# Kernel tuning notes

Measured on AMD Instinct MI355X. Metric: run time of the kernel, lower is better.

The kernel has to match this reference:

```python
import jax, jax.numpy as jnp
import numpy as np

N = 50000      # nodes
E = 1000000    # edges
NF = 5         # node_features
EF = 2         # edge_features
RS = 128       # rnn_size
RES = 32       # rnn_edge_size
H = 4          # heads
C = 16         # out_features
FIN = RS + RES # GAT in_channels
NEG_SLOPE = 0.2


def lstm_step(x, h, c, Wih, Whh, bih, bhh):
    # Single-step LSTM (torch gate order: i, f, g, o)
    g = x @ Wih.T + h @ Whh.T + bih + bhh
    i, f, gg, o = jnp.split(g, 4, axis=-1)
    i = jax.nn.sigmoid(i); f = jax.nn.sigmoid(f)
    gg = jnp.tanh(gg); o = jax.nn.sigmoid(o)
    c2 = f * c + i * gg
    return o * jnp.tanh(c2), c2


def setup_inputs() -> dict:
    key = jax.random.key(0)
    ks = jax.random.split(key, 20)
    p = lambda k, shape: (jax.random.normal(k, shape) * 0.1).astype(jnp.float32)
    return dict(
        x=jax.random.normal(ks[0], (N, NF), jnp.float32),
        edge_index=jax.random.randint(ks[1], (2, E), 0, N),
        edge_attr=jax.random.normal(ks[2], (E, EF), jnp.float32),
        h_node_h=p(ks[3], (N, RS)), h_node_c=p(ks[4], (N, RS)),
        h_edge_h=p(ks[5], (E, RES)), h_edge_c=p(ks[6], (E, RES)),
        Wih_n=p(ks[7], (4 * RS, NF)), Whh_n=p(ks[8], (4 * RS, RS)),
        bih_n=p(ks[9], (4 * RS,)), bhh_n=p(ks[10], (4 * RS,)),
        Wih_e=p(ks[11], (4 * RES, EF)), Whh_e=p(ks[12], (4 * RES, RES)),
        bih_e=p(ks[13], (4 * RES,)), bhh_e=p(ks[14], (4 * RES,)),
        W_gat=p(ks[15], (FIN, H * C)),
        att_src=p(ks[16], (H, C)), att_dst=p(ks[17], (H, C)),
        bias_gat=p(ks[18], (C,)),
    )


def reference(x, edge_index, edge_attr, h_node_h, h_node_c, h_edge_h, h_edge_c,
              Wih_n, Whh_n, bih_n, bhh_n, Wih_e, Whh_e, bih_e, bhh_e,
              W_gat, att_src, att_dst, bias_gat):
    n = x.shape[0]
    # --- edge history encoder: per-edge LSTM step + scatter-mean to dst nodes ---
    he, ce = lstm_step(edge_attr, h_edge_h, h_edge_c, Wih_e, Whh_e, bih_e, bhh_e)
    dst0 = edge_index[1]
    esum = jax.ops.segment_sum(he, dst0, num_segments=n)
    deg = jax.ops.segment_sum(jnp.ones((he.shape[0], 1), he.dtype), dst0, num_segments=n)
    edge_enc = esum / jnp.maximum(deg, 1.0)            # [N, RES]
    # --- node history encoder: per-node LSTM step ---
    hn, cn = lstm_step(x, h_node_h, h_node_c, Wih_n, Whh_n, bih_n, bhh_n)
    feat = jnp.concatenate([hn, edge_enc], axis=-1)    # [N, FIN]
    # --- GATConv (PyG v1 style, add_self_loops=True, concat=False) ---
    xl = (feat @ W_gat).reshape(n, H, C)               # [N, H, C]
    a_src = jnp.einsum('nhc,hc->nh', xl, att_src)
    a_dst = jnp.einsum('nhc,hc->nh', xl, att_dst)
    loops = jnp.arange(n)
    src = jnp.concatenate([edge_index[0], loops])
    dst = jnp.concatenate([edge_index[1], loops])
    alpha = jax.nn.leaky_relu(a_src[src] + a_dst[dst], NEG_SLOPE)  # [E+N, H]
    m = jax.ops.segment_max(alpha, dst, num_segments=n)
    ea = jnp.exp(alpha - m[dst])
    s = jax.ops.segment_sum(ea, dst, num_segments=n)
    w = ea / s[dst]                                     # segment softmax over dst
    out = jax.ops.segment_sum(xl[src] * w[:, :, None], dst, num_segments=n)  # [N,H,C]
    out = out.mean(axis=1) + bias_gat                   # concat=False -> head mean
    return (out, hn, cn, he, ce)
```

## Files before the change

### kernel.cpp

```cpp
#include <hip/hip_runtime.h>

#define CAP 128

typedef __attribute__((ext_vector_type(8))) short bf16x8;
typedef __attribute__((ext_vector_type(4))) float f32x4;

__device__ __forceinline__ float sigf(float x) {
    return __builtin_amdgcn_rcpf(1.0f + __expf(-x));
}
__device__ __forceinline__ float tanhfast(float x) {
    return 2.0f * __builtin_amdgcn_rcpf(1.0f + __expf(-2.0f * x)) - 1.0f;
}
__device__ __forceinline__ short bfr(float f) {
    unsigned u = __float_as_uint(f);
    unsigned r = (u + 0x7FFFu + ((u >> 16) & 1u)) >> 16;
    return (short)r;
}
__device__ __forceinline__ float bf2f(unsigned short u) {
    return __uint_as_float(((unsigned)u) << 16);
}
__device__ __forceinline__ bf16x8 cvt8(const float* p) {
    const float4* q = (const float4*)p;
    float4 u = q[0], v = q[1];
    bf16x8 r;
    r[0]=bfr(u.x); r[1]=bfr(u.y); r[2]=bfr(u.z); r[3]=bfr(u.w);
    r[4]=bfr(v.x); r[5]=bfr(v.y); r[6]=bfr(v.z); r[7]=bfr(v.w);
    return r;
}

__global__ void convert_kernel(
    const float* __restrict__ Whh_n, const float* __restrict__ Wih_n,
    const float* __restrict__ bih_n, const float* __restrict__ bhh_n,
    const float* __restrict__ Whh_e, const float* __restrict__ Wih_e,
    const float* __restrict__ bih_e, const float* __restrict__ bhh_e,
    const float* __restrict__ Wgat,
    unsigned short* __restrict__ WnF, unsigned short* __restrict__ WeF,
    unsigned short* __restrict__ WgF, int* __restrict__ cnt, int N)
{
    int i = blockIdx.x * 256 + threadIdx.x;
    if (i < N) cnt[i] = 0;
    if (i < 512 * 160) {
        int j = i & 7, unit = i >> 3;
        int lane = unit & 63, tk = unit >> 6;
        int tp = tk / 5, k4 = tk - tp * 5;
        int r = (tp & 3) * 128 + (tp >> 2) * 16 + (lane & 15);
        int k = k4 * 32 + (lane >> 4) * 8 + j;
        float v = (k < 128) ? Whh_n[r * 128 + k]
                : (k < 133) ? Wih_n[r * 5 + (k - 128)]
                : (k == 133) ? (bih_n[r] + bhh_n[r]) : 0.f;
        WnF[i] = (unsigned short)bfr(v);
    }
    if (i < 128 * 64) {
        int j = i & 7, unit = i >> 3;
        int lane = unit & 63, ts = unit >> 6;
        int t = ts >> 1, s = ts & 1;
        int r = t * 16 + (lane & 15);
        int k = s * 32 + (lane >> 4) * 8 + j;
        float v = (k < 32) ? Whh_e[r * 32 + k]
                : (k < 34) ? Wih_e[r * 2 + (k - 32)]
                : (k == 34) ? (bih_e[r] + bhh_e[r]) : 0.f;
        WeF[i] = (unsigned short)bfr(v);
    }
    if (i < 64 * 160) {
        int j = i & 7, unit = i >> 3;
        int lane = unit & 63, tk = unit >> 6;
        int t = tk / 5, k4 = tk - t * 5;
        int r = t * 16 + (lane & 15);
        int k = k4 * 32 + (lane >> 4) * 8 + j;
        WgF[i] = (unsigned short)bfr(Wgat[k * 64 + r]);
    }
}

__global__ void csr_fill_kernel(const int* __restrict__ dst, int* __restrict__ cnt,
                                int* __restrict__ eid, int E)
{
    int e = blockIdx.x * blockDim.x + threadIdx.x;
    if (e >= E) return;
    int d = dst[e];
    int k = atomicAdd(cnt + d, 1);
    if (k < CAP) eid[(size_t)d * CAP + k] = e;
}

__global__ __launch_bounds__(256, 4) void edge_lstm_mfma(
    const float* __restrict__ eattr, const float* __restrict__ h_in, const float* __restrict__ c_in,
    const unsigned short* __restrict__ WeF,
    float* __restrict__ he_out, float* __restrict__ ce_out, int E)
{
    __shared__ float Gall[4][16 * 132];
    __shared__ unsigned short Hall[4][16 * 40];
    const int lane = threadIdx.x & 63, wave = threadIdx.x >> 6;
    const int lr = lane & 15, lg = lane >> 4;
    const int tile = blockIdx.x * 4 + wave;
    if (tile * 16 >= E) return;
    float* G = Gall[wave];
    unsigned short* H = Hall[wave];

    const size_t dwbase = (size_t)tile * 512;
    const f32x4 hA = *(const f32x4*)(h_in + dwbase + lane * 4);
    const f32x4 hB = *(const f32x4*)(h_in + dwbase + 256 + lane * 4);
    const f32x4 cA = *(const f32x4*)(c_in + dwbase + lane * 4);
    const f32x4 cB = *(const f32x4*)(c_in + dwbase + 256 + lane * 4);
    float ea0 = 0.f, ea1 = 0.f;
    if (lg == 0) {
        ea0 = eattr[(size_t)(tile * 16 + lr) * 2];
        ea1 = eattr[(size_t)(tile * 16 + lr) * 2 + 1];
    }

    const bf16x8* Wv = (const bf16x8*)WeF;
    bf16x8 wa0[8], wa1[8];
    #pragma unroll
    for (int t = 0; t < 8; ++t) {
        wa0[t] = Wv[(t * 2 + 0) * 64 + lane];
        wa1[t] = Wv[(t * 2 + 1) * 64 + lane];
    }

    {
        const int e = lane >> 3, c4 = (lane & 7) * 4;
        ushort4 pa, pb;
        pa.x = (unsigned short)bfr(hA[0]); pa.y = (unsigned short)bfr(hA[1]);
        pa.z = (unsigned short)bfr(hA[2]); pa.w = (unsigned short)bfr(hA[3]);
        pb.x = (unsigned short)bfr(hB[0]); pb.y = (unsigned short)bfr(hB[1]);
        pb.z = (unsigned short)bfr(hB[2]); pb.w = (unsigned short)bfr(hB[3]);
        *(ushort4*)(H + e * 40 + c4)       = pa;
        *(ushort4*)(H + (8 + e) * 40 + c4) = pb;
    }
    bf16x8 b0 = *(const bf16x8*)(H + lr * 40 + lg * 8);
    bf16x8 b1 = {0,0,0,0,0,0,0,0};
    if (lg == 0) {
        b1[0] = bfr(ea0); b1[1] = bfr(ea1); b1[2] = (short)0x3F80;
    }

    f32x4 acc[8];
    #pragma unroll
    for (int t = 0; t < 8; ++t) {
        f32x4 v = {0, 0, 0, 0};
        v = __builtin_amdgcn_mfma_f32_16x16x32_bf16(wa0[t], b0, v, 0, 0, 0);
        v = __builtin_amdgcn_mfma_f32_16x16x32_bf16(wa1[t], b1, v, 0, 0, 0);
        acc[t] = v;
    }

    #pragma unroll
    for (int u = 0; u < 8; ++u) {
        const int col = (u >> 1) * 32 + (u & 1) * 16 + lg * 4;
        *(f32x4*)(G + lr * 132 + col) = acc[u];
    }

    const int e = lane >> 3, jq = (lane & 7) * 4;
    #pragma unroll
    for (int part = 0; part < 2; ++part) {
        const float* gr = G + (part * 8 + e) * 132;
        const f32x4 gi = *(const f32x4*)(gr + jq);
        const f32x4 gf = *(const f32x4*)(gr + 32 + jq);
        const f32x4 gg = *(const f32x4*)(gr + 64 + jq);
        const f32x4 go = *(const f32x4*)(gr + 96 + jq);
        const f32x4 cold = part ? cB : cA;
        f32x4 cres, hres;
        #pragma unroll
        for (int q = 0; q < 4; ++q) {
            float c2 = sigf(gf[q]) * cold[q] + sigf(gi[q]) * tanhfast(gg[q]);
            cres[q] = c2;
            hres[q] = sigf(go[q]) * tanhfast(c2);
        }
        __builtin_nontemporal_store(cres, (f32x4*)(ce_out + dwbase + part * 256 + lane * 4));
        *(f32x4*)(he_out + dwbase + part * 256 + lane * 4) = hres;
    }
}

__global__ __launch_bounds__(256) void node_lstm_mfma(
    const float* __restrict__ x, const float* __restrict__ h_in, const float* __restrict__ c_in,
    const unsigned short* __restrict__ WnF,
    float* __restrict__ hn_out, float* __restrict__ cn_out, int N)
{
    const int lane = threadIdx.x & 63, wave = threadIdx.x >> 6;
    const int nbase = blockIdx.x * 64 + wave * 16;
    if (nbase >= N) return;
    const int lr = lane & 15, lg = lane >> 4;
    const int node = nbase + lr;
    bf16x8 b[5];
    const float* hp = h_in + (size_t)node * 128 + lg * 8;
    b[0] = cvt8(hp); b[1] = cvt8(hp + 32); b[2] = cvt8(hp + 64); b[3] = cvt8(hp + 96);
    bf16x8 bx = {0,0,0,0,0,0,0,0};
    if (lg == 0) {
        const float* xp = x + (size_t)node * 5;
        bx[0]=bfr(xp[0]); bx[1]=bfr(xp[1]); bx[2]=bfr(xp[2]); bx[3]=bfr(xp[3]); bx[4]=bfr(xp[4]);
        bx[5] = (short)0x3F80;
    }
    b[4] = bx;
    const bf16x8* Wv = (const bf16x8*)WnF;
    #pragma unroll
    for (int u = 0; u < 8; ++u) {
        f32x4 acc[4];
        #pragma unroll
        for (int g = 0; g < 4; ++g) {
            const bf16x8* ap = Wv + (u * 4 + g) * 320 + lane;
            f32x4 v = {0, 0, 0, 0};
            #pragma unroll
            for (int k4 = 0; k4 < 5; ++k4)
                v = __builtin_amdgcn_mfma_f32_16x16x32_bf16(ap[k4 * 64], b[k4], v, 0, 0, 0);
            acc[g] = v;
        }
        const int jb = u * 16 + lg * 4;
        f32x4 cold = *(const f32x4*)(c_in + (size_t)node * 128 + jb);
        f32x4 cres, hres;
        #pragma unroll
        for (int q = 0; q < 4; ++q) {
            float c2 = sigf(acc[1][q]) * cold[q] + sigf(acc[0][q]) * tanhfast(acc[2][q]);
            cres[q] = c2;
            hres[q] = sigf(acc[3][q]) * tanhfast(c2);
        }
        __builtin_nontemporal_store(cres, (f32x4*)(cn_out + (size_t)node * 128 + jb));
        *(f32x4*)(hn_out + (size_t)node * 128 + jb) = hres;
    }
}

__global__ __launch_bounds__(256) void enc_gatxl_kernel(
    const int* __restrict__ cnt, const int* __restrict__ eid, const float* __restrict__ he,
    const float* __restrict__ hn, const unsigned short* __restrict__ WgF,
    const float* __restrict__ attS, const float* __restrict__ attD,
    unsigned short* __restrict__ xlb, float* __restrict__ asrc, float* __restrict__ adst, int N)
{
    __shared__ float encs[64 * 36];
    const int lane = threadIdx.x & 63, wave = threadIdx.x >> 6;
    const int nbase = blockIdx.x * 64 + wave * 16;
    if (nbase >= N) return;
    const int half = lane >> 5, hl = lane & 31;
    const int g4 = hl >> 3, l8 = hl & 7;
    for (int t = 0; t < 16; t += 2) {
        const int node = nbase + t + half;
        const int c = cnt[node];
        const int m = min(c, CAP);
        const int* el = eid + (size_t)node * CAP;
        f32x4 acc = {0, 0, 0, 0};
        for (int i = g4; i < m; i += 4)
            acc += *(const f32x4*)(he + (size_t)el[i] * 32 + l8 * 4);
        #pragma unroll
        for (int off = 8; off <= 16; off <<= 1) {
            acc[0] += __shfl_xor(acc[0], off);
            acc[1] += __shfl_xor(acc[1], off);
            acc[2] += __shfl_xor(acc[2], off);
            acc[3] += __shfl_xor(acc[3], off);
        }
        if (g4 == 0) {
            float inv = 1.0f / fmaxf((float)c, 1.0f);
            f32x4 r; r[0]=acc[0]*inv; r[1]=acc[1]*inv; r[2]=acc[2]*inv; r[3]=acc[3]*inv;
            *(f32x4*)(&encs[(wave * 16 + t + half) * 36 + l8 * 4]) = r;
        }
    }
    const int lr = lane & 15, lg = lane >> 4;
    const int node = nbase + lr;
    bf16x8 b[5];
    const float* hp = hn + (size_t)node * 128 + lg * 8;
    b[0] = cvt8(hp); b[1] = cvt8(hp + 32); b[2] = cvt8(hp + 64); b[3] = cvt8(hp + 96);
    b[4] = cvt8(&encs[(wave * 16 + lr) * 36 + lg * 8]);
    const bf16x8* Wv = (const bf16x8*)WgF;
    #pragma unroll
    for (int t = 0; t < 4; ++t) {
        const bf16x8* ap = Wv + t * 320 + lane;
        f32x4 v = {0, 0, 0, 0};
        #pragma unroll
        for (int k4 = 0; k4 < 5; ++k4)
            v = __builtin_amdgcn_mfma_f32_16x16x32_bf16(ap[k4 * 64], b[k4], v, 0, 0, 0);
        ushort4 pk;
        pk.x = (unsigned short)bfr(v[0]); pk.y = (unsigned short)bfr(v[1]);
        pk.z = (unsigned short)bfr(v[2]); pk.w = (unsigned short)bfr(v[3]);
        *(ushort4*)(xlb + (size_t)node * 64 + t * 16 + lg * 4) = pk;
        const f32x4 ws = *(const f32x4*)(attS + t * 16 + lg * 4);
        const f32x4 wd = *(const f32x4*)(attD + t * 16 + lg * 4);
        float p1 = v[0]*ws[0] + v[1]*ws[1] + v[2]*ws[2] + v[3]*ws[3];
        float p2 = v[0]*wd[0] + v[1]*wd[1] + v[2]*wd[2] + v[3]*wd[3];
        p1 += __shfl_xor(p1, 16); p2 += __shfl_xor(p2, 16);
        p1 += __shfl_xor(p1, 32); p2 += __shfl_xor(p2, 32);
        if (lg == 0) {
            asrc[(size_t)node * 4 + t] = p1;
            adst[(size_t)node * 4 + t] = p2;
        }
    }
}

__global__ __launch_bounds__(256) void gat_node_kernel(
    const int* __restrict__ cnt, const int* __restrict__ eid,
    const int* __restrict__ src_idx,
    const float* __restrict__ asrc, const float* __restrict__ adst,
    const unsigned short* __restrict__ xlb, const float* __restrict__ bias,
    float* __restrict__ out, int N)
{
    const int wid = (blockIdx.x * blockDim.x + threadIdx.x) >> 6;
    const int lane = threadIdx.x & 63;
    if (wid >= N) return;
    const int n = wid;
    const int m = min(cnt[n], CAP);
    const int h = lane >> 4, c16 = lane & 15;
    const int nslot = (m + 15) >> 4;
    const float ad = adst[n * 4 + h];
    float aself = asrc[n * 4 + h] + ad;
    aself = aself > 0.f ? aself : 0.2f * aself;
    const int* el = eid + (size_t)n * CAP;
    int   ss[8];
    float aa[8];
    float mx = aself;
    #pragma unroll
    for (int k = 0; k < 8; ++k) {
        if (k >= nslot) break;
        int i = k * 16 + c16;
        if (i < m) {
            int s = src_idx[el[i]];
            float a = asrc[s * 4 + h] + ad;
            a = a > 0.f ? a : 0.2f * a;
            ss[k] = s; aa[k] = a;
            mx = fmaxf(mx, a);
        } else { ss[k] = 0; aa[k] = -1e30f; }
    }
    #pragma unroll
    for (int off = 1; off < 16; off <<= 1) mx = fmaxf(mx, __shfl_xor(mx, off));
    float ea[8];
    float p = 0.f;
    #pragma unroll
    for (int k = 0; k < 8; ++k) {
        if (k >= nslot) break;
        ea[k] = __expf(aa[k] - mx);
        p += ea[k];
    }
    #pragma unroll
    for (int off = 1; off < 16; off <<= 1) p += __shfl_xor(p, off);
    float eself = __expf(aself - mx);
    float sacc = eself + p;
    float oacc = eself * bf2f(xlb[(size_t)n * 64 + lane]);
    const int grp = lane & 48;
    #pragma unroll
    for (int k = 0; k < 8; ++k) {
        if (k >= nslot) break;
        const int lim = min(16, m - k * 16);
        #pragma unroll 4
        for (int cc = 0; cc < lim; ++cc) {
            int srcl = grp | cc;
            float w = __shfl(ea[k], srcl);
            int   s = __shfl(ss[k], srcl);
            oacc += w * bf2f(xlb[(size_t)s * 64 + lane]);
        }
    }
    float r = oacc / sacc;
    r += __shfl_xor(r, 16);
    r += __shfl_xor(r, 32);
    if (lane < 16) out[(size_t)n * 16 + lane] = 0.25f * r + bias[lane];
}

extern "C" void kernel_launch(void* const* d_in, const int* in_sizes, int n_in,
                              void* d_out, int out_size, void* d_ws, size_t ws_size,
                              hipStream_t stream)
{
    const float* x     = (const float*)d_in[0];
    const int*   ei    = (const int*)  d_in[1];
    const float* eattr = (const float*)d_in[2];
    const float* hn_h  = (const float*)d_in[3];
    const float* hn_c  = (const float*)d_in[4];
    const float* he_h  = (const float*)d_in[5];
    const float* he_c  = (const float*)d_in[6];
    const float* Wih_n = (const float*)d_in[7];
    const float* Whh_n = (const float*)d_in[8];
    const float* bih_n = (const float*)d_in[9];
    const float* bhh_n = (const float*)d_in[10];
    const float* Wih_e = (const float*)d_in[11];
    const float* Whh_e = (const float*)d_in[12];
    const float* bih_e = (const float*)d_in[13];
    const float* bhh_e = (const float*)d_in[14];
    const float* W_gat = (const float*)d_in[15];
    const float* attS  = (const float*)d_in[16];
    const float* attD  = (const float*)d_in[17];
    const float* biasG = (const float*)d_in[18];

    const int N = in_sizes[0] / 5;
    const int E = in_sizes[2] / 2;

    float* out = (float*)d_out;
    float* hn  = out + (size_t)N * 16;
    float* cn  = hn  + (size_t)N * 128;
    float* he  = cn  + (size_t)N * 128;
    float* ce  = he  + (size_t)E * 32;

    char* p = (char*)d_ws;
    size_t off = 0;
    auto take = [&](size_t bytes) -> void* {
        void* r = p + off;
        off = (off + bytes + 255) & ~(size_t)255;
        return r;
    };
    int*   cnt  = (int*)  take((size_t)N * 4);
    int*   eid  = (int*)  take((size_t)N * CAP * 4);
    unsigned short* xlb = (unsigned short*)take((size_t)N * 64 * 2);
    float* asrc = (float*)take((size_t)N * 4 * 4);
    float* adst = (float*)take((size_t)N * 4 * 4);
    unsigned short* WnF = (unsigned short*)take(512 * 160 * 2);
    unsigned short* WeF = (unsigned short*)take(128 * 64 * 2);
    unsigned short* WgF = (unsigned short*)take(64 * 160 * 2);

    convert_kernel<<<(512 * 160 + 255) / 256, 256, 0, stream>>>(
        Whh_n, Wih_n, bih_n, bhh_n, Whh_e, Wih_e, bih_e, bhh_e, W_gat,
        WnF, WeF, WgF, cnt, N);
    csr_fill_kernel<<<(E + 255) / 256, 256, 0, stream>>>(ei + E, cnt, eid, E);
    edge_lstm_mfma<<<(E + 63) / 64, 256, 0, stream>>>(
        eattr, he_h, he_c, WeF, he, ce, E);
    node_lstm_mfma<<<(N + 63) / 64, 256, 0, stream>>>(
        x, hn_h, hn_c, WnF, hn, cn, N);
    enc_gatxl_kernel<<<(N + 63) / 64, 256, 0, stream>>>(
        cnt, eid, he, hn, WgF, attS, attD, xlb, asrc, adst, N);
    gat_node_kernel<<<(N + 3) / 4, 256, 0, stream>>>(
        cnt, eid, ei, asrc, adst, xlb, biasG, out, N);
}
```

Baseline: 367.2 us.

## Make edge LSTM kernel persistent with register prefetch of next tile

Turns the edge LSTM kernel into a persistent grid-stride kernel with a fixed 768 blocks. Each wave loads its weight fragments once and prefetches the next tile's h, c and edge attributes into registers while computing the current tile. This is meant to amortize weight loads and hide global memory latency. It raises register pressure, so occupancy is lowered to 3 blocks per SM, and it relies on E being a multiple of 16, since E>>4 drops any partial tail tile.

```diff
diff --git a/kernel.cpp b/kernel.cpp
--- a/kernel.cpp
+++ b/kernel.cpp
@@ -81,7 +81,7 @@
     if (k < CAP) eid[(size_t)d * CAP + k] = e;
 }
 
-__global__ __launch_bounds__(256, 4) void edge_lstm_mfma(
+__global__ __launch_bounds__(256, 3) void edge_lstm_mfma(
     const float* __restrict__ eattr, const float* __restrict__ h_in, const float* __restrict__ c_in,
     const unsigned short* __restrict__ WeF,
     float* __restrict__ he_out, float* __restrict__ ce_out, int E)
@@ -90,21 +90,12 @@
     __shared__ unsigned short Hall[4][16 * 40];
     const int lane = threadIdx.x & 63, wave = threadIdx.x >> 6;
     const int lr = lane & 15, lg = lane >> 4;
-    const int tile = blockIdx.x * 4 + wave;
-    if (tile * 16 >= E) return;
+    const int T = E >> 4;
+    const int nwaves = gridDim.x * 4;
+    const int wid = blockIdx.x * 4 + wave;
+    if (wid >= T) return;
     float* G = Gall[wave];
     unsigned short* H = Hall[wave];
-
-    const size_t dwbase = (size_t)tile * 512;
-    const f32x4 hA = *(const f32x4*)(h_in + dwbase + lane * 4);
-    const f32x4 hB = *(const f32x4*)(h_in + dwbase + 256 + lane * 4);
-    const f32x4 cA = *(const f32x4*)(c_in + dwbase + lane * 4);
-    const f32x4 cB = *(const f32x4*)(c_in + dwbase + 256 + lane * 4);
-    float ea0 = 0.f, ea1 = 0.f;
-    if (lg == 0) {
-        ea0 = eattr[(size_t)(tile * 16 + lr) * 2];
-        ea1 = eattr[(size_t)(tile * 16 + lr) * 2 + 1];
-    }
 
     const bf16x8* Wv = (const bf16x8*)WeF;
     bf16x8 wa0[8], wa1[8];
@@ -114,55 +105,86 @@
         wa1[t] = Wv[(t * 2 + 1) * 64 + lane];
     }
 
+    f32x4 phA, phB, pcA, pcB; float pea0 = 0.f, pea1 = 0.f;
     {
-        const int e = lane >> 3, c4 = (lane & 7) * 4;
-        ushort4 pa, pb;
-        pa.x = (unsigned short)bfr(hA[0]); pa.y = (unsigned short)bfr(hA[1]);
-        pa.z = (unsigned short)bfr(hA[2]); pa.w = (unsigned short)bfr(hA[3]);
-        pb.x = (unsigned short)bfr(hB[0]); pb.y = (unsigned short)bfr(hB[1]);
-        pb.z = (unsigned short)bfr(hB[2]); pb.w = (unsigned short)bfr(hB[3]);
-        *(ushort4*)(H + e * 40 + c4)       = pa;
-        *(ushort4*)(H + (8 + e) * 40 + c4) = pb;
-    }
-    bf16x8 b0 = *(const bf16x8*)(H + lr * 40 + lg * 8);
-    bf16x8 b1 = {0,0,0,0,0,0,0,0};
-    if (lg == 0) {
-        b1[0] = bfr(ea0); b1[1] = bfr(ea1); b1[2] = (short)0x3F80;
-    }
-
-    f32x4 acc[8];
-    #pragma unroll
-    for (int t = 0; t < 8; ++t) {
-        f32x4 v = {0, 0, 0, 0};
-        v = __builtin_amdgcn_mfma_f32_16x16x32_bf16(wa0[t], b0, v, 0, 0, 0);
-        v = __builtin_amdgcn_mfma_f32_16x16x32_bf16(wa1[t], b1, v, 0, 0, 0);
-        acc[t] = v;
-    }
-
-    #pragma unroll
-    for (int u = 0; u < 8; ++u) {
-        const int col = (u >> 1) * 32 + (u & 1) * 16 + lg * 4;
-        *(f32x4*)(G + lr * 132 + col) = acc[u];
-    }
-
-    const int e = lane >> 3, jq = (lane & 7) * 4;
-    #pragma unroll
-    for (int part = 0; part < 2; ++part) {
-        const float* gr = G + (part * 8 + e) * 132;
-        const f32x4 gi = *(const f32x4*)(gr + jq);
-        const f32x4 gf = *(const f32x4*)(gr + 32 + jq);
-        const f32x4 gg = *(const f32x4*)(gr + 64 + jq);
-        const f32x4 go = *(const f32x4*)(gr + 96 + jq);
-        const f32x4 cold = part ? cB : cA;
-        f32x4 cres, hres;
-        #pragma unroll
-        for (int q = 0; q < 4; ++q) {
-            float c2 = sigf(gf[q]) * cold[q] + sigf(gi[q]) * tanhfast(gg[q]);
-            cres[q] = c2;
-            hres[q] = sigf(go[q]) * tanhfast(c2);
-        }
-        __builtin_nontemporal_store(cres, (f32x4*)(ce_out + dwbase + part * 256 + lane * 4));
-        *(f32x4*)(he_out + dwbase + part * 256 + lane * 4) = hres;
+        const size_t dwb = (size_t)wid * 512;
+        phA = *(const f32x4*)(h_in + dwb + lane * 4);
+        phB = *(const f32x4*)(h_in + dwb + 256 + lane * 4);
+        pcA = *(const f32x4*)(c_in + dwb + lane * 4);
+        pcB = *(const f32x4*)(c_in + dwb + 256 + lane * 4);
+        if (lg == 0) {
+            pea0 = eattr[(size_t)(wid * 16 + lr) * 2];
+            pea1 = eattr[(size_t)(wid * 16 + lr) * 2 + 1];
+        }
+    }
+
+    for (int t = wid; t < T; t += nwaves) {
+        const f32x4 hA = phA, hB = phB, cA = pcA, cB = pcB;
+        const float ea0 = pea0, ea1 = pea1;
+        const size_t dwbase = (size_t)t * 512;
+        const int tn = t + nwaves;
+        if (tn < T) {
+            const size_t dwb = (size_t)tn * 512;
+            phA = *(const f32x4*)(h_in + dwb + lane * 4);
+            phB = *(const f32x4*)(h_in + dwb + 256 + lane * 4);
+            pcA = *(const f32x4*)(c_in + dwb + lane * 4);
+            pcB = *(const f32x4*)(c_in + dwb + 256 + lane * 4);
+            if (lg == 0) {
+                pea0 = eattr[(size_t)(tn * 16 + lr) * 2];
+                pea1 = eattr[(size_t)(tn * 16 + lr) * 2 + 1];
+            }
+        }
+
+        {
+            const int e = lane >> 3, c4 = (lane & 7) * 4;
+            ushort4 pa, pb;
+            pa.x = (unsigned short)bfr(hA[0]); pa.y = (unsigned short)bfr(hA[1]);
+            pa.z = (unsigned short)bfr(hA[2]); pa.w = (unsigned short)bfr(hA[3]);
+            pb.x = (unsigned short)bfr(hB[0]); pb.y = (unsigned short)bfr(hB[1]);
+            pb.z = (unsigned short)bfr(hB[2]); pb.w = (unsigned short)bfr(hB[3]);
+            *(ushort4*)(H + e * 40 + c4)       = pa;
+            *(ushort4*)(H + (8 + e) * 40 + c4) = pb;
+        }
+        bf16x8 b0 = *(const bf16x8*)(H + lr * 40 + lg * 8);
+        bf16x8 b1 = {0,0,0,0,0,0,0,0};
+        if (lg == 0) {
+            b1[0] = bfr(ea0); b1[1] = bfr(ea1); b1[2] = (short)0x3F80;
+        }
+
+        f32x4 acc[8];
+        #pragma unroll
+        for (int tt = 0; tt < 8; ++tt) {
+            f32x4 v = {0, 0, 0, 0};
+            v = __builtin_amdgcn_mfma_f32_16x16x32_bf16(wa0[tt], b0, v, 0, 0, 0);
+            v = __builtin_amdgcn_mfma_f32_16x16x32_bf16(wa1[tt], b1, v, 0, 0, 0);
+            acc[tt] = v;
+        }
+
+        #pragma unroll
+        for (int u = 0; u < 8; ++u) {
+            const int col = (u >> 1) * 32 + (u & 1) * 16 + lg * 4;
+            *(f32x4*)(G + lr * 132 + col) = acc[u];
+        }
+
+        const int e = lane >> 3, jq = (lane & 7) * 4;
+        #pragma unroll
+        for (int part = 0; part < 2; ++part) {
+            const float* gr = G + (part * 8 + e) * 132;
+            const f32x4 gi = *(const f32x4*)(gr + jq);
+            const f32x4 gf = *(const f32x4*)(gr + 32 + jq);
+            const f32x4 gg = *(const f32x4*)(gr + 64 + jq);
+            const f32x4 go = *(const f32x4*)(gr + 96 + jq);
+            const f32x4 cold = part ? cB : cA;
+            f32x4 cres, hres;
+            #pragma unroll
+            for (int q = 0; q < 4; ++q) {
+                float c2 = sigf(gf[q]) * cold[q] + sigf(gi[q]) * tanhfast(gg[q]);
+                cres[q] = c2;
+                hres[q] = sigf(go[q]) * tanhfast(c2);
+            }
+            __builtin_nontemporal_store(cres, (f32x4*)(ce_out + dwbase + part * 256 + lane * 4));
+            *(f32x4*)(he_out + dwbase + part * 256 + lane * 4) = hres;
+        }
     }
 }
 
@@ -397,7 +419,7 @@
         Whh_n, Wih_n, bih_n, bhh_n, Whh_e, Wih_e, bih_e, bhh_e, W_gat,
         WnF, WeF, WgF, cnt, N);
     csr_fill_kernel<<<(E + 255) / 256, 256, 0, stream>>>(ei + E, cnt, eid, E);
-    edge_lstm_mfma<<<(E + 63) / 64, 256, 0, stream>>>(
+    edge_lstm_mfma<<<768, 256, 0, stream>>>(
         eattr, he_h, he_c, WeF, he, ce, E);
     node_lstm_mfma<<<(N + 63) / 64, 256, 0, stream>>>(
         x, hn_h, hn_c, WnF, hn, cn, N);
```

New measurement: 361.3 us. Within noise of the previous version (-1.6%).
